# Kernel optimization log

Hardware: AMD Instinct MI355X
Metric: run time of the kernel (lower is better)

## Reference

```python
import jax, jax.numpy as jnp
import numpy as np

IN_FEATURES = 4096
OUT_FEATURES = 4096
TOKENS = 8192


def setup_inputs() -> dict:
    key = jax.random.key(0)
    kx, kw, kb = jax.random.split(key, 3)
    x = jax.random.normal(kx, (TOKENS, IN_FEATURES), dtype=jnp.float32)
    # Simulate the offline quantization: a float weight quantized to 2-bit signed {-2,-1,0,1}
    w_f = jax.random.normal(kw, (OUT_FEATURES, IN_FEATURES), dtype=jnp.float32) * 0.02
    max_val = jnp.max(jnp.abs(w_f))
    scale = (max_val / 1.5 + 1e-8).astype(jnp.float32)
    weight_q = jnp.clip(jnp.round(w_f / scale), -2, 1).astype(jnp.int8)
    bias = jax.random.normal(kb, (OUT_FEATURES,), dtype=jnp.float32) * 0.01
    return {"x": x, "weight_q": weight_q, "scale": scale, "bias": bias}


def reference(x, weight_q, scale, bias):
    # Dequantize 2-bit weights then standard linear: y = x @ W^T + b
    w = weight_q.astype(jnp.float32) * scale  # [out, in]
    return jnp.einsum('ti,oi->to', x, w) + bias
```

## Files before the change

### kernel.cpp

```cpp
#include <hip/hip_runtime.h>
#include <stdint.h>

#define TOKENS 8192
#define INF    4096
#define OUTF   4096
#define BM     256
#define BN     128
#define NTIL   64

typedef __bf16 bf16x8 __attribute__((ext_vector_type(8)));
typedef float  f32x4  __attribute__((ext_vector_type(4)));
typedef unsigned short ushort_t;

__device__ __forceinline__ unsigned short f2bf(float f) {
  union { float f; unsigned int u; } v;
  v.f = f;
  unsigned int r = v.u + 0x7fffu + ((v.u >> 16) & 1u);
  return (unsigned short)(r >> 16);
}

__global__ void l2b_conv_x(const float* __restrict__ x,
                           unsigned short* __restrict__ xb, int n4) {
  int idx = blockIdx.x * blockDim.x + threadIdx.x;
  int stride = gridDim.x * blockDim.x;
  for (int i = idx; i < n4; i += stride) {
    float4 v = reinterpret_cast<const float4*>(x)[i];
    ushort4 o;
    o.x = f2bf(v.x); o.y = f2bf(v.y); o.z = f2bf(v.z); o.w = f2bf(v.w);
    reinterpret_cast<ushort4*>(xb)[i] = o;
  }
}

__global__ void l2b_conv_w(const int* __restrict__ w,
                           unsigned short* __restrict__ wb, int n4) {
  int idx = blockIdx.x * blockDim.x + threadIdx.x;
  int stride = gridDim.x * blockDim.x;
  for (int i = idx; i < n4; i += stride) {
    int4 v = reinterpret_cast<const int4*>(w)[i];
    ushort4 o;
    o.x = f2bf((float)v.x); o.y = f2bf((float)v.y);
    o.z = f2bf((float)v.z); o.w = f2bf((float)v.w);
    reinterpret_cast<ushort4*>(wb)[i] = o;
  }
}

__device__ __forceinline__ void gload_lds16(const ushort_t* g, ushort_t* l) {
  auto gp = reinterpret_cast<__attribute__((address_space(1))) unsigned int*>(
      reinterpret_cast<uintptr_t>(g));
  auto lp = reinterpret_cast<__attribute__((address_space(3))) unsigned int*>(
      reinterpret_cast<uintptr_t>(l));
  __builtin_amdgcn_global_load_lds(gp, lp, 16, 0, 0);
}

__device__ __forceinline__ int swz(int b) { return b ^ (((b >> 9) & 1) << 5); }

__device__ __forceinline__ bf16x8 ldsRd(const ushort_t* slot, int row, int colb) {
  int off = (row << 7) | colb;
  off ^= ((off >> 9) & 1) << 5;
  return *reinterpret_cast<const bf16x8*>(
      reinterpret_cast<const char*>(slot) + off);
}

__device__ __forceinline__ f32x4 mfma(bf16x8 a, bf16x8 b, f32x4 c) {
  return __builtin_amdgcn_mfma_f32_16x16x32_bf16(a, b, c, 0, 0, 0);
}

#define LGKM8() do { asm volatile("s_waitcnt lgkmcnt(8)" ::: "memory"); \
                     __builtin_amdgcn_sched_barrier(0); } while (0)
#define LGKM0() do { asm volatile("s_waitcnt lgkmcnt(0)" ::: "memory"); \
                     __builtin_amdgcn_sched_barrier(0); } while (0)

template <int VMB, bool STG, bool PRER>
__device__ __forceinline__ void ktile(
    const ushort_t* __restrict__ A, const ushort_t* __restrict__ B,
    int rowBlk, int colBlk, int t,
    const ushort_t* rA, const ushort_t* rB,
    const ushort_t* nA, const ushort_t* nB,
    ushort_t* sA, ushort_t* sB,
    bf16x8 (&a0)[4], bf16x8 (&b0)[4], f32x4 (&acc)[4][4],
    int ar, int brw, int fk, int wid, const int (&geA)[4], const int (&geB)[2]) {
  if (STG) {
    const ushort_t* gA = A + (size_t)rowBlk * INF + (t + 2) * 64;
    const ushort_t* gB = B + (size_t)colBlk * INF + (t + 2) * 64;
#pragma unroll
    for (int r = 0; r < 4; ++r)
      gload_lds16(gA + geA[r], sA + r * 4096 + wid * 512);
#pragma unroll
    for (int r = 0; r < 2; ++r)
      gload_lds16(gB + geB[r], sB + r * 4096 + wid * 512);
  }
  bf16x8 a1[4], b1[4];
#pragma unroll
  for (int m = 0; m < 4; ++m) a1[m] = ldsRd(rA, ar + m * 16, 64 + fk * 16);
#pragma unroll
  for (int n = 0; n < 4; ++n) b1[n] = ldsRd(rB, brw + n * 16, 64 + fk * 16);
  LGKM8();
  __builtin_amdgcn_s_setprio(1);
#pragma unroll
  for (int m = 0; m < 4; ++m)
#pragma unroll
    for (int n = 0; n < 4; ++n)
      acc[m][n] = mfma(a0[m], b0[n], acc[m][n]);
  __builtin_amdgcn_s_setprio(0);
  if (VMB == 6) asm volatile("s_waitcnt vmcnt(6)" ::: "memory");
  if (VMB == 0) asm volatile("s_waitcnt vmcnt(0)" ::: "memory");
  __builtin_amdgcn_s_barrier();
  if (PRER) {
#pragma unroll
    for (int m = 0; m < 4; ++m) a0[m] = ldsRd(nA, ar + m * 16, fk * 16);
#pragma unroll
    for (int n = 0; n < 4; ++n) b0[n] = ldsRd(nB, brw + n * 16, fk * 16);
  }
  if (PRER) { LGKM8(); } else { LGKM0(); }
  __builtin_amdgcn_s_setprio(1);
#pragma unroll
  for (int m = 0; m < 4; ++m)
#pragma unroll
    for (int n = 0; n < 4; ++n)
      acc[m][n] = mfma(a1[m], b1[n], acc[m][n]);
  __builtin_amdgcn_s_setprio(0);
}

__global__ __launch_bounds__(512, 2) void l2b_gemmP(
    const ushort_t* __restrict__ A, const ushort_t* __restrict__ B,
    const float* __restrict__ scale, const float* __restrict__ bias,
    float* __restrict__ C) {
  extern __shared__ ushort_t smem[];
  ushort_t* slA[3] = { smem, smem + 24576, smem + 49152 };
  ushort_t* slB[3] = { smem + 16384, smem + 40960, smem + 65536 };

  const int tid  = threadIdx.x;
  const int lane = tid & 63;
  const int wid  = tid >> 6;
  const int wm = wid >> 1, wn = wid & 1;
  const int fr = lane & 15, fk = lane >> 4;
  const int ar  = wm * 64 + fr;
  const int brw = wn * 64 + fr;

  const int bid = (int)blockIdx.x;
  const int idx = (bid & 7) * 128 + (bid >> 3);
  const int bm = idx >> 5, bn = idx & 31;
  const int rowBlk = bm * BM, colBlk = bn * BN;

  int geA[4], geB[2];
#pragma unroll
  for (int r = 0; r < 4; ++r) {
    const int p = swz(r * 8192 + tid * 16);
    geA[r] = (p >> 7) * INF + ((p & 127) >> 1);
  }
#pragma unroll
  for (int r = 0; r < 2; ++r) {
    const int p = swz(r * 8192 + tid * 16);
    geB[r] = (p >> 7) * INF + ((p & 127) >> 1);
  }

  {
    const ushort_t* gA = A + (size_t)rowBlk * INF;
    const ushort_t* gB = B + (size_t)colBlk * INF;
#pragma unroll
    for (int r = 0; r < 4; ++r) gload_lds16(gA + geA[r], slA[0] + r * 4096 + wid * 512);
#pragma unroll
    for (int r = 0; r < 2; ++r) gload_lds16(gB + geB[r], slB[0] + r * 4096 + wid * 512);
#pragma unroll
    for (int r = 0; r < 4; ++r) gload_lds16(gA + 64 + geA[r], slA[1] + r * 4096 + wid * 512);
#pragma unroll
    for (int r = 0; r < 2; ++r) gload_lds16(gB + 64 + geB[r], slB[1] + r * 4096 + wid * 512);
  }
  asm volatile("s_waitcnt vmcnt(6)" ::: "memory");
  __builtin_amdgcn_s_barrier();

  bf16x8 a0[4], b0[4];
#pragma unroll
  for (int m = 0; m < 4; ++m) a0[m] = ldsRd(slA[0], ar + m * 16, fk * 16);
#pragma unroll
  for (int n = 0; n < 4; ++n) b0[n] = ldsRd(slB[0], brw + n * 16, fk * 16);

  f32x4 acc[4][4] = {};

  const ushort_t *rA = slA[0], *rB = slB[0], *nA = slA[1], *nB = slB[1];
  ushort_t *sA = slA[2], *sB = slB[2];

#pragma unroll 1
  for (int t = 0; t < NTIL - 2; ++t) {
    ktile<6, true, true>(A, B, rowBlk, colBlk, t,
        rA, rB, nA, nB, sA, sB, a0, b0, acc, ar, brw, fk, wid, geA, geB);
    const ushort_t* tA = rA; const ushort_t* tB = rB;
    rA = nA; rB = nB; nA = sA; nB = sB;
    sA = const_cast<ushort_t*>(tA); sB = const_cast<ushort_t*>(tB);
  }
  ktile<0, false, true>(A, B, rowBlk, colBlk, NTIL - 2,
      rA, rB, nA, nB, sA, sB, a0, b0, acc, ar, brw, fk, wid, geA, geB);
  {
    const ushort_t* tA = rA; const ushort_t* tB = rB;
    rA = nA; rB = nB; nA = sA; nB = sB;
    sA = const_cast<ushort_t*>(tA); sB = const_cast<ushort_t*>(tB);
  }
  ktile<-1, false, false>(A, B, rowBlk, colBlk, NTIL - 1,
      rA, rB, nA, nB, sA, sB, a0, b0, acc, ar, brw, fk, wid, geA, geB);

  const float s = scale[0];
#pragma unroll
  for (int n = 0; n < 4; ++n) {
    const int col = colBlk + wn * 64 + n * 16 + fr;
    const float bv = bias[col];
#pragma unroll
    for (int m = 0; m < 4; ++m) {
      const int row = rowBlk + wm * 64 + m * 16 + fk * 4;
#pragma unroll
      for (int j = 0; j < 4; ++j)
        C[(size_t)(row + j) * OUTF + col] = acc[m][n][j] * s + bv;
    }
  }
}

__global__ __launch_bounds__(256) void l2b_gemm(
    const ushort_t* __restrict__ A, const ushort_t* __restrict__ B,
    const float* __restrict__ scale, const float* __restrict__ bias,
    float* __restrict__ C) {
  constexpr int K = INF;
  constexpr int N = OUTF;
  __shared__ __align__(16) ushort_t ldsA[128 * 32];
  __shared__ __align__(16) ushort_t ldsB[128 * 32];
  const int tid = threadIdx.x;
  const int lane = tid & 63;
  const int wid = tid >> 6;
  const int wm = wid >> 1, wn = wid & 1;
  const int bm = blockIdx.x >> 5, bn = blockIdx.x & 31;
  const int row0 = bm * 128, col0 = bn * 128;
  const int lr = lane >> 4, lc = lane & 15;
  f32x4 acc[4][4] = {};
  for (int k0 = 0; k0 < K; k0 += 32) {
#pragma unroll
    for (int i = 0; i < 2; ++i) {
      const int idx = i * 256 + tid;
      const int r = idx >> 2;
      const int c = (idx & 3) * 8;
      ushort_t* lbaseA = ldsA + i * 2048 + wid * 512;
      ushort_t* lbaseB = ldsB + i * 2048 + wid * 512;
      gload_lds16(A + (size_t)(row0 + r) * K + (k0 + c), lbaseA);
      gload_lds16(B + (size_t)(col0 + r) * K + (k0 + c), lbaseB);
    }
    __syncthreads();
    bf16x8 af[4], bfr[4];
#pragma unroll
    for (int m = 0; m < 4; ++m)
      af[m] = *reinterpret_cast<const bf16x8*>(
          &ldsA[(wm * 64 + m * 16 + lc) * 32 + lr * 8]);
#pragma unroll
    for (int n = 0; n < 4; ++n)
      bfr[n] = *reinterpret_cast<const bf16x8*>(
          &ldsB[(wn * 64 + n * 16 + lc) * 32 + lr * 8]);
#pragma unroll
    for (int m = 0; m < 4; ++m)
#pragma unroll
      for (int n = 0; n < 4; ++n)
        acc[m][n] = mfma(af[m], bfr[n], acc[m][n]);
    __syncthreads();
  }
  const float s = scale[0];
#pragma unroll
  for (int n = 0; n < 4; ++n) {
    const int col = col0 + wn * 64 + n * 16 + lc;
    const float bv = bias[col];
#pragma unroll
    for (int m = 0; m < 4; ++m) {
      const int row = row0 + wm * 64 + m * 16 + lr * 4;
#pragma unroll
      for (int i = 0; i < 4; ++i)
        C[(size_t)(row + i) * N + col] = acc[m][n][i] * s + bv;
    }
  }
}

__global__ void l2b_naive(const float* __restrict__ x, const int* __restrict__ w,
                          const float* __restrict__ scale,
                          const float* __restrict__ bias,
                          float* __restrict__ out) {
  const int o = blockIdx.x * blockDim.x + threadIdx.x;
  if (o >= TOKENS * OUTF) return;
  const int t = o / OUTF;
  const int n = o - t * OUTF;
  const float* xr = x + (size_t)t * INF;
  const int* wr = w + (size_t)n * INF;
  float acc = 0.f;
  for (int k = 0; k < INF; ++k) acc += xr[k] * (float)wr[k];
  out[o] = acc * scale[0] + bias[n];
}

extern "C" void kernel_launch(void* const* d_in, const int* in_sizes, int n_in,
                              void* d_out, int out_size, void* d_ws, size_t ws_size,
                              hipStream_t stream) {
  const float* x     = (const float*)d_in[0];
  const int*   wq    = (const int*)d_in[1];
  const float* scale = (const float*)d_in[2];
  const float* bias  = (const float*)d_in[3];
  float* out = (float*)d_out;

  const size_t xbytes = (size_t)TOKENS * INF * 2;
  const size_t wbytes = (size_t)OUTF * INF * 2;

  if (ws_size >= xbytes + wbytes) {
    unsigned short* xb = (unsigned short*)d_ws;
    unsigned short* wb = (unsigned short*)((char*)d_ws + xbytes);
    l2b_conv_x<<<2048, 256, 0, stream>>>(x, xb, TOKENS * INF / 4);
    l2b_conv_w<<<2048, 256, 0, stream>>>(wq, wb, OUTF * INF / 4);

    hipError_t e = hipFuncSetAttribute(
        reinterpret_cast<const void*>(l2b_gemmP),
        hipFuncAttributeMaxDynamicSharedMemorySize, 147456);
    if (e == hipSuccess) {
      l2b_gemmP<<<dim3((TOKENS / BM) * (OUTF / BN)), 512, 147456, stream>>>(
          xb, wb, scale, bias, out);
    } else {
      l2b_gemm<<<dim3((TOKENS / 128) * (OUTF / 128)), 256, 0, stream>>>(
          xb, wb, scale, bias, out);
    }
  } else {
    l2b_naive<<<(TOKENS * OUTF + 255) / 256, 256, 0, stream>>>(
        x, wq, scale, bias, out);
  }
}
```

Baseline: 309.5 us.

## Replace 256x128 triple-buffered GEMM with 128x128 double-buffered 4-wave kernel

Swaps the 512-thread, 256x128 tile, triple-buffered LDS pipeline for a 256-thread, 128x128 tile kernel with two LDS buffers. The LDS XOR swizzle becomes row-based, and all fragment reads for a K-tile are issued up front. Staging of the next tile is moved between the two MFMA halves, and LDS use drops from 144KB to 64KB to fit more blocks per CU. The cost is lower data reuse per block and a shallower prefetch pipeline with more barriers.

```diff
diff --git a/kernel.cpp b/kernel.cpp
--- a/kernel.cpp
+++ b/kernel.cpp
@@ -4,9 +4,7 @@
 #define TOKENS 8192
 #define INF    4096
 #define OUTF   4096
-#define BM     256
-#define BN     128
-#define NTIL   64
+#define NT     64
 
 typedef __bf16 bf16x8 __attribute__((ext_vector_type(8)));
 typedef float  f32x4  __attribute__((ext_vector_type(4)));
@@ -52,151 +50,122 @@
   __builtin_amdgcn_global_load_lds(gp, lp, 16, 0, 0);
 }
 
-__device__ __forceinline__ int swz(int b) { return b ^ (((b >> 9) & 1) << 5); }
-
 __device__ __forceinline__ bf16x8 ldsRd(const ushort_t* slot, int row, int colb) {
-  int off = (row << 7) | colb;
-  off ^= ((off >> 9) & 1) << 5;
+  int off = ((row << 7) | colb) ^ ((row & 7) << 4);
   return *reinterpret_cast<const bf16x8*>(
       reinterpret_cast<const char*>(slot) + off);
 }
 
+__device__ __forceinline__ void stage_slot(const ushort_t* __restrict__ src,
+                                           ushort_t* slot, int wid,
+                                           const int (&ge)[4]) {
+#pragma unroll
+  for (int r = 0; r < 4; ++r)
+    gload_lds16(src + ge[r], slot + r * 2048 + wid * 512);
+}
+
 __device__ __forceinline__ f32x4 mfma(bf16x8 a, bf16x8 b, f32x4 c) {
   return __builtin_amdgcn_mfma_f32_16x16x32_bf16(a, b, c, 0, 0, 0);
 }
 
-#define LGKM8() do { asm volatile("s_waitcnt lgkmcnt(8)" ::: "memory"); \
-                     __builtin_amdgcn_sched_barrier(0); } while (0)
-#define LGKM0() do { asm volatile("s_waitcnt lgkmcnt(0)" ::: "memory"); \
-                     __builtin_amdgcn_sched_barrier(0); } while (0)
-
-template <int VMB, bool STG, bool PRER>
+template <int VMB, bool STG>
 __device__ __forceinline__ void ktile(
     const ushort_t* __restrict__ A, const ushort_t* __restrict__ B,
     int rowBlk, int colBlk, int t,
     const ushort_t* rA, const ushort_t* rB,
-    const ushort_t* nA, const ushort_t* nB,
-    ushort_t* sA, ushort_t* sB,
-    bf16x8 (&a0)[4], bf16x8 (&b0)[4], f32x4 (&acc)[4][4],
-    int ar, int brw, int fk, int wid, const int (&geA)[4], const int (&geB)[2]) {
+    ushort_t* wA, ushort_t* wB,
+    f32x4 (&acc)[4][4], int ar, int br, int fkq, int wid, const int (&ge)[4]) {
+  bf16x8 a[4][2], b[4][2];
+#pragma unroll
+  for (int m = 0; m < 4; ++m) {
+    a[m][0] = ldsRd(rA, ar + m * 16, fkq);
+    a[m][1] = ldsRd(rA, ar + m * 16, 64 + fkq);
+  }
+#pragma unroll
+  for (int n = 0; n < 4; ++n) {
+    b[n][0] = ldsRd(rB, br + n * 16, fkq);
+    b[n][1] = ldsRd(rB, br + n * 16, 64 + fkq);
+  }
+  asm volatile("s_waitcnt lgkmcnt(0)" ::: "memory");
+  __builtin_amdgcn_sched_barrier(0);
+  __builtin_amdgcn_s_setprio(1);
+#pragma unroll
+  for (int m = 0; m < 4; ++m)
+#pragma unroll
+    for (int n = 0; n < 4; ++n)
+      acc[m][n] = mfma(a[m][0], b[n][0], acc[m][n]);
+  __builtin_amdgcn_s_setprio(0);
+  __builtin_amdgcn_s_barrier();
   if (STG) {
-    const ushort_t* gA = A + (size_t)rowBlk * INF + (t + 2) * 64;
-    const ushort_t* gB = B + (size_t)colBlk * INF + (t + 2) * 64;
-#pragma unroll
-    for (int r = 0; r < 4; ++r)
-      gload_lds16(gA + geA[r], sA + r * 4096 + wid * 512);
-#pragma unroll
-    for (int r = 0; r < 2; ++r)
-      gload_lds16(gB + geB[r], sB + r * 4096 + wid * 512);
-  }
-  bf16x8 a1[4], b1[4];
-#pragma unroll
-  for (int m = 0; m < 4; ++m) a1[m] = ldsRd(rA, ar + m * 16, 64 + fk * 16);
-#pragma unroll
-  for (int n = 0; n < 4; ++n) b1[n] = ldsRd(rB, brw + n * 16, 64 + fk * 16);
-  LGKM8();
+    stage_slot(A + (size_t)rowBlk * INF + (t + 2) * 64, wA, wid, ge);
+    stage_slot(B + (size_t)colBlk * INF + (t + 2) * 64, wB, wid, ge);
+  }
   __builtin_amdgcn_s_setprio(1);
 #pragma unroll
   for (int m = 0; m < 4; ++m)
 #pragma unroll
     for (int n = 0; n < 4; ++n)
-      acc[m][n] = mfma(a0[m], b0[n], acc[m][n]);
+      acc[m][n] = mfma(a[m][1], b[n][1], acc[m][n]);
   __builtin_amdgcn_s_setprio(0);
-  if (VMB == 6) asm volatile("s_waitcnt vmcnt(6)" ::: "memory");
+  if (VMB == 8) asm volatile("s_waitcnt vmcnt(8)" ::: "memory");
   if (VMB == 0) asm volatile("s_waitcnt vmcnt(0)" ::: "memory");
   __builtin_amdgcn_s_barrier();
-  if (PRER) {
-#pragma unroll
-    for (int m = 0; m < 4; ++m) a0[m] = ldsRd(nA, ar + m * 16, fk * 16);
-#pragma unroll
-    for (int n = 0; n < 4; ++n) b0[n] = ldsRd(nB, brw + n * 16, fk * 16);
-  }
-  if (PRER) { LGKM8(); } else { LGKM0(); }
-  __builtin_amdgcn_s_setprio(1);
-#pragma unroll
-  for (int m = 0; m < 4; ++m)
-#pragma unroll
-    for (int n = 0; n < 4; ++n)
-      acc[m][n] = mfma(a1[m], b1[n], acc[m][n]);
-  __builtin_amdgcn_s_setprio(0);
-}
-
-__global__ __launch_bounds__(512, 2) void l2b_gemmP(
+}
+
+__global__ __launch_bounds__(256, 2) void l2b_gemmD(
     const ushort_t* __restrict__ A, const ushort_t* __restrict__ B,
     const float* __restrict__ scale, const float* __restrict__ bias,
     float* __restrict__ C) {
   extern __shared__ ushort_t smem[];
-  ushort_t* slA[3] = { smem, smem + 24576, smem + 49152 };
-  ushort_t* slB[3] = { smem + 16384, smem + 40960, smem + 65536 };
+  ushort_t* sA0 = smem;          ushort_t* sA1 = smem + 8192;
+  ushort_t* sB0 = smem + 16384;  ushort_t* sB1 = smem + 24576;
 
   const int tid  = threadIdx.x;
   const int lane = tid & 63;
   const int wid  = tid >> 6;
   const int wm = wid >> 1, wn = wid & 1;
   const int fr = lane & 15, fk = lane >> 4;
-  const int ar  = wm * 64 + fr;
-  const int brw = wn * 64 + fr;
+  const int ar = wm * 64 + fr;
+  const int br = wn * 64 + fr;
+  const int fkq = fk * 16;
 
   const int bid = (int)blockIdx.x;
-  const int idx = (bid & 7) * 128 + (bid >> 3);
+  const int idx = (bid & 7) * 256 + (bid >> 3);
   const int bm = idx >> 5, bn = idx & 31;
-  const int rowBlk = bm * BM, colBlk = bn * BN;
-
-  int geA[4], geB[2];
+  const int rowBlk = bm * 128, colBlk = bn * 128;
+
+  int ge[4];
 #pragma unroll
   for (int r = 0; r < 4; ++r) {
-    const int p = swz(r * 8192 + tid * 16);
-    geA[r] = (p >> 7) * INF + ((p & 127) >> 1);
-  }
-#pragma unroll
-  for (int r = 0; r < 2; ++r) {
-    const int p = swz(r * 8192 + tid * 16);
-    geB[r] = (p >> 7) * INF + ((p & 127) >> 1);
-  }
-
-  {
-    const ushort_t* gA = A + (size_t)rowBlk * INF;
-    const ushort_t* gB = B + (size_t)colBlk * INF;
-#pragma unroll
-    for (int r = 0; r < 4; ++r) gload_lds16(gA + geA[r], slA[0] + r * 4096 + wid * 512);
-#pragma unroll
-    for (int r = 0; r < 2; ++r) gload_lds16(gB + geB[r], slB[0] + r * 4096 + wid * 512);
-#pragma unroll
-    for (int r = 0; r < 4; ++r) gload_lds16(gA + 64 + geA[r], slA[1] + r * 4096 + wid * 512);
-#pragma unroll
-    for (int r = 0; r < 2; ++r) gload_lds16(gB + 64 + geB[r], slB[1] + r * 4096 + wid * 512);
-  }
-  asm volatile("s_waitcnt vmcnt(6)" ::: "memory");
+    const int P = r * 4096 + tid * 16;
+    const int row = P >> 7;
+    const int col = (P & 127) ^ ((row & 7) << 4);
+    ge[r] = row * INF + (col >> 1);
+  }
+
+  stage_slot(A + (size_t)rowBlk * INF,      sA0, wid, ge);
+  stage_slot(B + (size_t)colBlk * INF,      sB0, wid, ge);
+  stage_slot(A + (size_t)rowBlk * INF + 64, sA1, wid, ge);
+  stage_slot(B + (size_t)colBlk * INF + 64, sB1, wid, ge);
+  asm volatile("s_waitcnt vmcnt(8)" ::: "memory");
   __builtin_amdgcn_s_barrier();
 
-  bf16x8 a0[4], b0[4];
-#pragma unroll
-  for (int m = 0; m < 4; ++m) a0[m] = ldsRd(slA[0], ar + m * 16, fk * 16);
-#pragma unroll
-  for (int n = 0; n < 4; ++n) b0[n] = ldsRd(slB[0], brw + n * 16, fk * 16);
-
   f32x4 acc[4][4] = {};
 
-  const ushort_t *rA = slA[0], *rB = slB[0], *nA = slA[1], *nB = slB[1];
-  ushort_t *sA = slA[2], *sB = slB[2];
-
 #pragma unroll 1
-  for (int t = 0; t < NTIL - 2; ++t) {
-    ktile<6, true, true>(A, B, rowBlk, colBlk, t,
-        rA, rB, nA, nB, sA, sB, a0, b0, acc, ar, brw, fk, wid, geA, geB);
-    const ushort_t* tA = rA; const ushort_t* tB = rB;
-    rA = nA; rB = nB; nA = sA; nB = sB;
-    sA = const_cast<ushort_t*>(tA); sB = const_cast<ushort_t*>(tB);
-  }
-  ktile<0, false, true>(A, B, rowBlk, colBlk, NTIL - 2,
-      rA, rB, nA, nB, sA, sB, a0, b0, acc, ar, brw, fk, wid, geA, geB);
-  {
-    const ushort_t* tA = rA; const ushort_t* tB = rB;
-    rA = nA; rB = nB; nA = sA; nB = sB;
-    sA = const_cast<ushort_t*>(tA); sB = const_cast<ushort_t*>(tB);
-  }
-  ktile<-1, false, false>(A, B, rowBlk, colBlk, NTIL - 1,
-      rA, rB, nA, nB, sA, sB, a0, b0, acc, ar, brw, fk, wid, geA, geB);
+  for (int t = 0; t < NT - 2; ++t) {
+    const int p = t & 1;
+    const ushort_t* rA = p ? sA1 : sA0;
+    const ushort_t* rB = p ? sB1 : sB0;
+    ushort_t* wA = p ? sA1 : sA0;
+    ushort_t* wB = p ? sB1 : sB0;
+    ktile<8, true>(A, B, rowBlk, colBlk, t,
+        rA, rB, wA, wB, acc, ar, br, fkq, wid, ge);
+  }
+  ktile<0, false>(A, B, rowBlk, colBlk, NT - 2,
+      sA0, sB0, sA0, sB0, acc, ar, br, fkq, wid, ge);
+  ktile<-1, false>(A, B, rowBlk, colBlk, NT - 1,
+      sA1, sB1, sA1, sB1, acc, ar, br, fkq, wid, ge);
 
   const float s = scale[0];
 #pragma unroll
@@ -306,10 +275,10 @@
     l2b_conv_w<<<2048, 256, 0, stream>>>(wq, wb, OUTF * INF / 4);
 
     hipError_t e = hipFuncSetAttribute(
-        reinterpret_cast<const void*>(l2b_gemmP),
-        hipFuncAttributeMaxDynamicSharedMemorySize, 147456);
+        reinterpret_cast<const void*>(l2b_gemmD),
+        hipFuncAttributeMaxDynamicSharedMemorySize, 65536);
     if (e == hipSuccess) {
-      l2b_gemmP<<<dim3((TOKENS / BM) * (OUTF / BN)), 512, 147456, stream>>>(
+      l2b_gemmD<<<dim3((TOKENS / 128) * (OUTF / 128)), 256, 65536, stream>>>(
           xb, wb, scale, bias, out);
     } else {
       l2b_gemm<<<dim3((TOKENS / 128) * (OUTF / 128)), 256, 0, stream>>>(
```

Result: slower. 368.6 us (+19.1%).
